# Kernel tuning notes

Measured on AMD Instinct MI355X. Metric: run time of the kernel, lower is better.

The kernel has to match this reference:

```python
import jax, jax.numpy as jnp
import numpy as np

H, K, V, F = 8, 64, 192, 192  # heads, key_size, value_size, num_position_features


def central_mask_features(distances, feature_size, seq_length):
    # distances: [L] float; returns [L, feature_size]
    pow_rate = np.exp(np.log(seq_length + 1) / feature_size).astype('float32')
    center_widths = jnp.power(pow_rate, jnp.arange(1, feature_size + 1, dtype=jnp.float32)) - 1.0
    return (center_widths[None, :] > jnp.abs(distances)[:, None]).astype(jnp.float32)


def positional_features(distances, feature_size, seq_length, symmetric=False):
    num_components = 1 if symmetric else 2
    emb = central_mask_features(distances, feature_size // num_components, seq_length)
    if not symmetric:
        emb = jnp.concatenate([emb, jnp.sign(distances)[:, None] * emb], axis=-1)
    return emb  # [L, feature_size]


def relative_shift(x):
    # x: [B, H, T1, T2] with T2 = 2*T1 - 1 -> [B, H, T1, T1]
    b, h, t1, t2 = x.shape
    x = jnp.pad(x, ((0, 0), (0, 0), (0, 0), (1, 0)))  # [B,H,T1,T2+1]
    x = x.reshape(b, h, t2 + 1, t1)[:, :, 1:, :]      # drop first row
    x = x.reshape(b, h, t1, t2)
    return x[..., : (t2 + 1) // 2]


def setup_inputs() -> dict:
    key = jax.random.key(0)
    ks = jax.random.split(key, 9)
    B, T, C = 2, 1536, 1536
    s = 1.0 / np.sqrt(C).astype('float32')
    return {
        'inputs': jax.random.normal(ks[0], (B, T, C), jnp.float32),
        'Wq': jax.random.normal(ks[1], (C, H * K), jnp.float32) * s,
        'Wk': jax.random.normal(ks[2], (C, H * K), jnp.float32) * s,
        'Wv': jax.random.normal(ks[3], (C, H * V), jnp.float32) * s,
        'Wrk': jax.random.normal(ks[4], (F, H * K), jnp.float32) * (1.0 / np.sqrt(F).astype('float32')),
        'We': jax.random.normal(ks[5], (H * V, H * V), jnp.float32) * (1.0 / np.sqrt(H * V).astype('float32')),
        'be': jnp.zeros((H * V,), jnp.float32),
        'r_w_bias': jax.random.normal(ks[6], (1, H, 1, K), jnp.float32) * 0.1,
        'r_r_bias': jax.random.normal(ks[7], (1, H, 1, K), jnp.float32) * 0.1,
    }


def reference(inputs, Wq, Wk, Wv, Wrk, We, be, r_w_bias, r_r_bias):
    B, T, C = inputs.shape

    def heads(x, d):  # [B,T,H*d] -> [B,H,T,d]
        return x.reshape(B, T, H, d).transpose(0, 2, 1, 3)

    q = heads(inputs @ Wq, K) * (K ** -0.5)
    k = heads(inputs @ Wk, K)
    v = heads(inputs @ Wv, V)

    # content logits: (q + r_w_bias) k^T -> [B,H,T,T]
    content_logits = jnp.einsum('bhqk,bhmk->bhqm', q + r_w_bias, k)

    # relative position logits
    distances = jnp.arange(-T + 1, T, dtype=jnp.float32)  # [2T-1]
    pe = positional_features(distances, F, T, symmetric=False)  # [2T-1, F]
    r_k = (pe @ Wrk).reshape(2 * T - 1, H, K).transpose(1, 0, 2)  # [H, 2T-1, K]
    rel_logits = jnp.einsum('bhqk,hmk->bhqm', q + r_r_bias, r_k)  # [B,H,T,2T-1]
    rel_logits = relative_shift(rel_logits)  # [B,H,T,T]

    logits = content_logits + rel_logits
    attn = jax.nn.softmax(logits, axis=-1)
    out = jnp.einsum('bhqm,bhmv->bhqv', attn, v)  # [B,H,T,V]
    out = out.transpose(0, 2, 1, 3).reshape(B, T, H * V)
    return out @ We + be
```

## Files before the change

### kernel.cpp

```cpp
#include <hip/hip_runtime.h>
#include <math.h>

#define HB 8
#define KD 64
#define VD 192
#define BT 2
#define TT 1536
#define CC 1536
#define HK (HB*KD)
#define HV (HB*VD)
#define QKVP 2560

typedef float f32x4 __attribute__((ext_vector_type(4)));
typedef __bf16 bf16x8 __attribute__((ext_vector_type(8)));
typedef uint uint2v __attribute__((ext_vector_type(2)));

static __device__ __forceinline__ ushort f2bf(float f) {
  union { float f; uint u; } v; v.f = f;
  uint r = (v.u + 0x7FFFu + ((v.u >> 16) & 1u)) >> 16;
  return (ushort)r;
}
static __device__ __forceinline__ float bf2f(ushort u) {
  union { uint u; float f; } v; v.u = ((uint)u) << 16; return v.f;
}

static __device__ __forceinline__ f32x4 mfma_bf(bf16x8 a, bf16x8 b, f32x4 c) {
  return __builtin_amdgcn_mfma_f32_16x16x32_bf16(a, b, c, 0, 0, 0);
}

static __device__ __forceinline__ void gload_lds16(const ushort* g, ushort* l) {
  __builtin_amdgcn_global_load_lds(
      (const __attribute__((address_space(1))) unsigned int*)g,
      (__attribute__((address_space(3))) unsigned int*)l, 16, 0, 0);
}

__device__ __forceinline__ void storeC(float* p, float v) { *p = v; }
__device__ __forceinline__ void storeC(ushort* p, float v) { *p = f2bf(v); }

__global__ __launch_bounds__(256) void cast_bf16(
    const float* __restrict__ in, ushort* __restrict__ out, int n4)
{
  for (int i = blockIdx.x*blockDim.x + threadIdx.x; i < n4; i += gridDim.x*blockDim.x) {
    float4 v = ((const float4*)in)[i];
    ushort4 o; o.x = f2bf(v.x); o.y = f2bf(v.y); o.z = f2bf(v.z); o.w = f2bf(v.w);
    ((ushort4*)out)[i] = o;
  }
}

__global__ void tcast(const float* __restrict__ in, ushort* __restrict__ out, int R, int C, float scale)
{
  __shared__ float tile[32][33];
  const int bx = blockIdx.x * 32;
  const int by = blockIdx.y * 32;
  const int tx = threadIdx.x, ty = threadIdx.y;
  #pragma unroll
  for (int i = 0; i < 4; ++i)
    tile[ty + i*8][tx] = in[(size_t)(by + ty + i*8)*C + bx + tx];
  __syncthreads();
  #pragma unroll
  for (int i = 0; i < 4; ++i)
    out[(size_t)(bx + ty + i*8)*R + by + tx] = f2bf(tile[tx][ty + i*8] * scale);
}

__global__ void vtrans(const ushort* __restrict__ in, ushort* __restrict__ out)
{
  __shared__ ushort tile[32][33];
  const int bx = blockIdx.x * 32;
  const int by = blockIdx.y * 32;
  const int tx = threadIdx.x, ty = threadIdx.y;
  #pragma unroll
  for (int i = 0; i < 4; ++i)
    tile[ty + i*8][tx] = in[(size_t)(by + ty + i*8)*QKVP + 1024 + bx + tx];
  __syncthreads();
  #pragma unroll
  for (int i = 0; i < 4; ++i)
    out[(size_t)(bx + ty + i*8)*(BT*TT) + by + tx] = tile[tx][ty + i*8];
}

template<bool WITH_BIAS, typename OutT>
__global__ __launch_bounds__(256) void gemm_bf16(
    const ushort* __restrict__ A, const ushort* __restrict__ Bt,
    const float* __restrict__ bias, OutT* __restrict__ C,
    int M, int N, int Kd)
{
  __shared__ __align__(16) ushort As[128*64];
  __shared__ __align__(16) ushort Bs[128*64];
  const int t = threadIdx.x;
  const int w = t >> 6, lane = t & 63;
  const int lrow = lane & 15, lk8 = lane >> 4;
  const int row0 = blockIdx.y * 128, col0 = blockIdx.x * 128;
  const int wr = (w >> 1) * 64, wc = (w & 1) * 64;

  f32x4 acc[4][4];
  #pragma unroll
  for (int m = 0; m < 4; ++m)
    #pragma unroll
    for (int n = 0; n < 4; ++n) acc[m][n] = (f32x4){0.f,0.f,0.f,0.f};

  for (int k0 = 0; k0 < Kd; k0 += 64) {
    __syncthreads();
    #pragma unroll
    for (int j = 0; j < 4; ++j) {
      const int c = (w*4 + j)*64 + lane;
      const int r = c >> 3, cp = c & 7;
      const int sc = cp ^ (r & 7);
      gload_lds16(A  + (size_t)(row0 + r)*Kd + k0 + sc*8, As + c*8);
      gload_lds16(Bt + (size_t)(col0 + r)*Kd + k0 + sc*8, Bs + c*8);
    }
    __syncthreads();
    bf16x8 af[4][2], bfv[4][2];
    #pragma unroll
    for (int m = 0; m < 4; ++m) {
      const int r = wr + m*16 + lrow;
      #pragma unroll
      for (int kh = 0; kh < 2; ++kh) {
        const int k8 = lk8 + kh*4;
        af[m][kh] = *(const bf16x8*)&As[r*64 + ((k8 ^ (r & 7)) << 3)];
      }
    }
    #pragma unroll
    for (int n = 0; n < 4; ++n) {
      const int r = wc + n*16 + lrow;
      #pragma unroll
      for (int kh = 0; kh < 2; ++kh) {
        const int k8 = lk8 + kh*4;
        bfv[n][kh] = *(const bf16x8*)&Bs[r*64 + ((k8 ^ (r & 7)) << 3)];
      }
    }
    #pragma unroll
    for (int m = 0; m < 4; ++m)
      #pragma unroll
      for (int n = 0; n < 4; ++n) {
        acc[m][n] = mfma_bf(af[m][0], bfv[n][0], acc[m][n]);
        acc[m][n] = mfma_bf(af[m][1], bfv[n][1], acc[m][n]);
      }
  }
  #pragma unroll
  for (int m = 0; m < 4; ++m)
    #pragma unroll
    for (int n = 0; n < 4; ++n) {
      const int cg = col0 + wc + n*16 + lrow;
      const float bb = WITH_BIAS ? bias[cg] : 0.f;
      #pragma unroll
      for (int r = 0; r < 4; ++r) {
        const int rg = row0 + wr + m*16 + lk8*4 + r;
        storeC(&C[(size_t)rg*N + cg], acc[m][n][r] + bb);
      }
    }
}

__global__ __launch_bounds__(256) void wrk_suffix(
    const float* __restrict__ Wrk, float* __restrict__ S1, float* __restrict__ S2)
{
  const int c = blockIdx.x*blockDim.x + threadIdx.x;
  float a1 = 0.f, a2 = 0.f;
  S1[96*HK + c] = 0.f; S2[96*HK + c] = 0.f;
  for (int i = 95; i >= 0; --i) {
    a1 += Wrk[i*HK + c];
    a2 += Wrk[(96 + i)*HK + c];
    S1[i*HK + c] = a1; S2[i*HK + c] = a2;
  }
}

__global__ __launch_bounds__(256) void relk_fill(
    const float* __restrict__ S1, const float* __restrict__ S2,
    const float* __restrict__ rrb, ushort* __restrict__ rk, float* __restrict__ c2g)
{
  __shared__ float cw[96];
  __shared__ float red[512];
  __shared__ int i0s;
  const int t = threadIdx.x;
  const int m = blockIdx.x;
  if (t < 96) {
    double pr = exp(log((double)(TT + 1)) / 96.0);
    float prf = (float)pr;
    cw[t] = (float)pow((double)prf, (double)(t + 1)) - 1.0f;
  }
  __syncthreads();
  const int d = m - (TT - 1);
  const float ad = fabsf((float)d);
  if (t == 0) {
    int i0 = 96;
    for (int i = 0; i < 96; ++i) if (cw[i] > ad) { i0 = i; break; }
    i0s = i0;
  }
  __syncthreads();
  const float sg = (d > 0) ? 1.f : (d < 0 ? -1.f : 0.f);
  const int i0 = i0s;
  for (int c = t; c < HK; c += 256) {
    const float val = S1[i0*HK + c] + sg * S2[i0*HK + c];
    const ushort vb = f2bf(val);
    rk[(size_t)m * HK + c] = vb;
    red[c] = bf2f(vb) * rrb[c];
  }
  __syncthreads();
  if (t < 8) {
    float s = 0.f;
    #pragma unroll 16
    for (int i = 0; i < 64; ++i) s += red[t*64 + i];
    c2g[(size_t)t*(2*TT - 1) + m] = s;
  }
}

__global__ __launch_bounds__(256) void c1_kernel(
    const ushort* __restrict__ qkv, const float* __restrict__ rwb, float* __restrict__ c1g)
{
  const int idx = blockIdx.x*256 + threadIdx.x;
  const int h = idx & 7, row = idx >> 3;
  const ushort* kr = &qkv[(size_t)row*QKVP + 512 + h*KD];
  float s = 0.f;
  #pragma unroll 16
  for (int c = 0; c < 64; ++c) s += bf2f(kr[c]) * rwb[h*KD + c];
  c1g[h*(BT*TT) + row] = s;
}

__global__ __launch_bounds__(256) void attn_mfma(
    const ushort* __restrict__ qkv, const ushort* __restrict__ vTg,
    const ushort* __restrict__ rk,
    const float* __restrict__ c1g, const float* __restrict__ c2g,
    ushort* __restrict__ aout)
{
  __shared__ __align__(16) ushort ktL[32*64];
  __shared__ __align__(16) ushort rkbL[64*64];
  __shared__ __align__(16) ushort vTl[192*64];
  __shared__ __align__(16) ushort Pl[32][40];
  __shared__ __align__(16) float S1[32][33];
  __shared__ __align__(16) float S2[32][66];
  __shared__ float c1s[32], c2s[64];
  __shared__ float corrl[32], linv[32];

  const int t = threadIdx.x;
  const int wv = t >> 6, lane = t & 63;
  const int lrow = lane & 15, lk8 = lane >> 4;
  const int bid = blockIdx.x;
  const int qt = bid % (TT/32);
  const int h  = (bid / (TT/32)) % HB;
  const int b  = bid / ((TT/32) * HB);
  const int q0 = qt * 32;

  bf16x8 af[2][2];
  #pragma unroll
  for (int rt = 0; rt < 2; ++rt)
    #pragma unroll
    for (int kh = 0; kh < 2; ++kh)
      af[rt][kh] = *(const bf16x8*)&qkv[((size_t)(b*TT) + q0 + rt*16 + lrow)*QKVP + h*KD + kh*32 + lk8*8];

  if (t < 32) ((uint*)rkbL)[63*32 + t] = 0;

  const int kc_r = t >> 3, kc_p = t & 7;
  const ushort* ksrc = qkv + (size_t)(b*TT + kc_r)*QKVP + 512 + h*KD + (kc_p ^ (kc_r & 7))*8;
  ushort* kdst = ktL + t*8;
  const ushort* rsrc[2]; ushort* rdst[2];
  #pragma unroll
  for (int W = 0; W < 2; ++W) {
    const int c = W*256 + t;
    const int rr = c >> 3, cp = c & 7;
    rsrc[W] = rk + (size_t)(TT - 32 - q0 + rr)*HK + h*KD + (cp ^ (rr & 7))*8;
    rdst[W] = rkbL + c*8;
  }
  const bool rval = t < 248;
  const ushort* vsrc[6]; ushort* vdst[6];
  #pragma unroll
  for (int W = 0; W < 6; ++W) {
    const int c = W*256 + t;
    const int vd = c >> 3, cpk = c & 7;
    vsrc[W] = vTg + (size_t)(h*VD + vd)*(BT*TT) + b*TT + (cpk ^ (vd & 7))*8;
    vdst[W] = vTl + c*8;
  }

  f32x4 acc[2][3];
  #pragma unroll
  for (int i = 0; i < 2; ++i)
    #pragma unroll
    for (int j = 0; j < 3; ++j) acc[i][j] = (f32x4){0.f, 0.f, 0.f, 0.f};
  float m_i = -1e30f, l_i = 0.f;
  const int r_s = t >> 3;
  const int vsl = t & 7;

  for (int kt0 = 0; kt0 < TT; kt0 += 32) {
    __syncthreads();
    gload_lds16(ksrc, kdst);                 ksrc += 32*QKVP;
    gload_lds16(rsrc[0], rdst[0]);           rsrc[0] += 32*HK;
    if (rval) gload_lds16(rsrc[1], rdst[1]); rsrc[1] += 32*HK;
    if ((kt0 & 32) == 0) {
      #pragma unroll
      for (int W = 0; W < 6; ++W) { gload_lds16(vsrc[W], vdst[W]); vsrc[W] += 64; }
    }
    const int mbase = kt0 - q0 + (TT - 32);
    if (t < 32) c1s[t] = c1g[h*(BT*TT) + b*TT + kt0 + t];
    else if (t >= 64 && t < 128) {
      const int m = t - 64;
      c2s[m] = (m < 63) ? c2g[(size_t)h*(2*TT - 1) + mbase + m] : 0.f;
    }
    asm volatile("s_waitcnt vmcnt(0)" ::: "memory");
    __syncthreads();
    {
      const int rt = wv >> 1, ct = wv & 1;
      const int jk = ct*16 + lrow;
      bf16x8 b0 = *(const bf16x8*)&ktL[jk*64 + ((lk8 ^ (jk & 7)) << 3)];
      bf16x8 b1 = *(const bf16x8*)&ktL[jk*64 + (((lk8 + 4) ^ (jk & 7)) << 3)];
      f32x4 c0 = (f32x4){0.f, 0.f, 0.f, 0.f};
      c0 = mfma_bf(af[rt][0], b0, c0);
      c0 = mfma_bf(af[rt][1], b1, c0);
      const float cadd = c1s[jk];
      #pragma unroll
      for (int r = 0; r < 4; ++r) S1[rt*16 + lk8*4 + r][jk] = c0[r] + cadd;
    }
    #pragma unroll
    for (int s2 = 0; s2 < 2; ++s2) {
      const int rt = wv >> 1, ct = (wv & 1)*2 + s2;
      const int j2 = ct*16 + lrow;
      bf16x8 b0 = *(const bf16x8*)&rkbL[j2*64 + ((lk8 ^ (j2 & 7)) << 3)];
      bf16x8 b1 = *(const bf16x8*)&rkbL[j2*64 + (((lk8 + 4) ^ (j2 & 7)) << 3)];
      f32x4 c0 = (f32x4){0.f, 0.f, 0.f, 0.f};
      c0 = mfma_bf(af[rt][0], b0, c0);
      c0 = mfma_bf(af[rt][1], b1, c0);
      const float cadd = c2s[j2];
      #pragma unroll
      for (int r = 0; r < 4; ++r) S2[rt*16 + lk8*4 + r][j2] = c0[r] + cadd;
    }
    __syncthreads();
    {
      float sv[4];
      #pragma unroll
      for (int i = 0; i < 4; ++i) {
        const int j = vsl*4 + i;
        sv[i] = S1[r_s][j] + S2[r_s][j - r_s + 31];
      }
      float lmax = fmaxf(fmaxf(sv[0], sv[1]), fmaxf(sv[2], sv[3]));
      #pragma unroll
      for (int s = 1; s < 8; s <<= 1) lmax = fmaxf(lmax, __shfl_xor(lmax, s, 64));
      const float m_new = fmaxf(m_i, lmax);
      const float corr = __expf(m_i - m_new);
      const float p0 = __expf(sv[0] - m_new), p1 = __expf(sv[1] - m_new);
      const float p2 = __expf(sv[2] - m_new), p3 = __expf(sv[3] - m_new);
      uint2v pw;
      pw.x = (uint)f2bf(p0) | ((uint)f2bf(p1) << 16);
      pw.y = (uint)f2bf(p2) | ((uint)f2bf(p3) << 16);
      *(uint2v*)&Pl[r_s][vsl*4] = pw;
      float lsum = (p0 + p1) + (p2 + p3);
      #pragma unroll
      for (int s = 1; s < 8; s <<= 1) lsum += __shfl_xor(lsum, s, 64);
      l_i = l_i * corr + lsum;
      m_i = m_new;
      if (vsl == 0) corrl[r_s] = corr;
    }
    __syncthreads();
    {
      const int kh4 = ((kt0 >> 5) & 1) * 4;
      float cr[2][4];
      #pragma unroll
      for (int rt = 0; rt < 2; ++rt)
        #pragma unroll
        for (int r = 0; r < 4; ++r) cr[rt][r] = corrl[rt*16 + lk8*4 + r];
      #pragma unroll
      for (int rt = 0; rt < 2; ++rt) {
        const bf16x8 pa = *(const bf16x8*)&Pl[rt*16 + lrow][lk8*8];
        #pragma unroll
        for (int cc = 0; cc < 3; ++cc) {
          const int rv = (3*wv + cc)*16 + lrow;
          const bf16x8 bv = *(const bf16x8*)&vTl[rv*64 + (((kh4 + lk8) ^ (rv & 7)) << 3)];
          f32x4 a = acc[rt][cc];
          #pragma unroll
          for (int r = 0; r < 4; ++r) a[r] *= cr[rt][r];
          acc[rt][cc] = mfma_bf(pa, bv, a);
        }
      }
    }
  }
  if (vsl == 0) linv[r_s] = 1.0f / l_i;
  __syncthreads();
  #pragma unroll
  for (int rt = 0; rt < 2; ++rt) {
    #pragma unroll
    for (int cc = 0; cc < 3; ++cc) {
      const int colg = (3*wv + cc)*16 + lrow;
      #pragma unroll
      for (int r = 0; r < 4; ++r) {
        const int rowg = rt*16 + lk8*4 + r;
        aout[((size_t)(b*TT) + q0 + rowg) * HV + h*VD + colg] = f2bf(acc[rt][cc][r] * linv[rowg]);
      }
    }
  }
}

extern "C" void kernel_launch(void* const* d_in, const int* in_sizes, int n_in,
                              void* d_out, int out_size, void* d_ws, size_t ws_size,
                              hipStream_t stream)
{
  const float* X   = (const float*)d_in[0];
  const float* Wq  = (const float*)d_in[1];
  const float* Wk  = (const float*)d_in[2];
  const float* Wv  = (const float*)d_in[3];
  const float* Wrk = (const float*)d_in[4];
  const float* We  = (const float*)d_in[5];
  const float* be  = (const float*)d_in[6];
  const float* rwb = (const float*)d_in[7];
  const float* rrb = (const float*)d_in[8];
  float* out = (float*)d_out;

  char* ws = (char*)d_ws;
  ushort* Xb    = (ushort*)ws;                       ws += (size_t)3072*1536*2;
  ushort* Wqkvt = (ushort*)ws;                       ws += (size_t)2560*1536*2;
  ushort* Wet   = (ushort*)ws;                       ws += (size_t)1536*1536*2;
  float*  S1b   = (float*)ws;                        ws += (size_t)97*512*4;
  float*  S2b   = (float*)ws;                        ws += (size_t)97*512*4;
  ushort* qkvb  = (ushort*)ws;                       ws += (size_t)3072*2560*2;
  ushort* vTgb  = (ushort*)ws;                       ws += (size_t)1536*3072*2;
  ushort* rkb   = (ushort*)ws;                       ws += (size_t)3071*512*2;
  float*  c1g   = (float*)ws;                        ws += (size_t)8*3072*4;
  float*  c2g   = (float*)ws;                        ws += (size_t)8*3071*4;
  ushort* ao    = (ushort*)ws;

  dim3 blk(256);
  cast_bf16<<<2048, blk, 0, stream>>>(X, Xb, (3072*1536)/4);
  tcast<<<dim3(512/32, 1536/32),  dim3(32,8), 0, stream>>>(Wq, Wqkvt,                      1536, 512,  0.125f);
  tcast<<<dim3(512/32, 1536/32),  dim3(32,8), 0, stream>>>(Wk, Wqkvt + (size_t)512*1536,   1536, 512,  1.0f);
  tcast<<<dim3(1536/32, 1536/32), dim3(32,8), 0, stream>>>(Wv, Wqkvt + (size_t)1024*1536,  1536, 1536, 1.0f);
  tcast<<<dim3(1536/32, 1536/32), dim3(32,8), 0, stream>>>(We, Wet, 1536, 1536, 1.0f);
  wrk_suffix<<<2, blk, 0, stream>>>(Wrk, S1b, S2b);
  relk_fill<<<dim3(2*TT - 1), blk, 0, stream>>>(S1b, S2b, rrb, rkb, c2g);
  gemm_bf16<false, ushort><<<dim3(20, 24), blk, 0, stream>>>(Xb, Wqkvt, nullptr, qkvb, 3072, QKVP, 1536);
  vtrans<<<dim3(1536/32, 3072/32), dim3(32,8), 0, stream>>>(qkvb, vTgb);
  c1_kernel<<<96, blk, 0, stream>>>(qkvb, rwb, c1g);
  attn_mfma<<<dim3(BT*HB*(TT/32)), blk, 0, stream>>>(qkvb, vTgb, rkb, c1g, c2g, ao);
  gemm_bf16<true, float><<<dim3(12, 24), blk, 0, stream>>>(ao, Wet, be, out, 3072, 1536, 1536);
}
```

Measured before the change: 226.0 us.

## Prefetch next K/rel-K tiles during softmax and defer softmax rescaling

Restructures the attention loop so the next key and relative-key tiles are issued right after the score MFMAs. Partial vmcnt waits let those loads overlap the softmax and PV stages, and raw s_barrier replaces the full __syncthreads. The c1/c2 bias terms are read directly into registers instead of being staged through LDS. Log2(e) is folded into the Q weights and biases so the kernel can use exp2f, and the running max is updated lazily (threshold 8), with the accumulator rescale skipped when no row changed. The lazy max lets the bf16 probabilities grow up to 2^8 before rescaling, and the hand-written waitcnt counts must match the issued load counts exactly.

```diff
diff --git a/kernel.cpp b/kernel.cpp
--- a/kernel.cpp
+++ b/kernel.cpp
@@ -10,6 +10,7 @@
 #define HK (HB*KD)
 #define HV (HB*VD)
 #define QKVP 2560
+#define LOG2E 1.44269504088896340736f
 
 typedef float f32x4 __attribute__((ext_vector_type(4)));
 typedef __bf16 bf16x8 __attribute__((ext_vector_type(8)));
@@ -198,7 +199,7 @@
     float s = 0.f;
     #pragma unroll 16
     for (int i = 0; i < 64; ++i) s += red[t*64 + i];
-    c2g[(size_t)t*(2*TT - 1) + m] = s;
+    c2g[(size_t)t*(2*TT - 1) + m] = s * LOG2E;
   }
 }
 
@@ -211,7 +212,7 @@
   float s = 0.f;
   #pragma unroll 16
   for (int c = 0; c < 64; ++c) s += bf2f(kr[c]) * rwb[h*KD + c];
-  c1g[h*(BT*TT) + row] = s;
+  c1g[h*(BT*TT) + row] = s * LOG2E;
 }
 
 __global__ __launch_bounds__(256) void attn_mfma(
@@ -224,9 +225,8 @@
   __shared__ __align__(16) ushort rkbL[64*64];
   __shared__ __align__(16) ushort vTl[192*64];
   __shared__ __align__(16) ushort Pl[32][40];
-  __shared__ __align__(16) float S1[32][33];
+  __shared__ __align__(16) float S1[32][34];
   __shared__ __align__(16) float S2[32][66];
-  __shared__ float c1s[32], c2s[64];
   __shared__ float corrl[32], linv[32];
 
   const int t = threadIdx.x;
@@ -250,14 +250,12 @@
   const int kc_r = t >> 3, kc_p = t & 7;
   const ushort* ksrc = qkv + (size_t)(b*TT + kc_r)*QKVP + 512 + h*KD + (kc_p ^ (kc_r & 7))*8;
   ushort* kdst = ktL + t*8;
-  const ushort* rsrc[2]; ushort* rdst[2];
-  #pragma unroll
-  for (int W = 0; W < 2; ++W) {
-    const int c = W*256 + t;
-    const int rr = c >> 3, cp = c & 7;
-    rsrc[W] = rk + (size_t)(TT - 32 - q0 + rr)*HK + h*KD + (cp ^ (rr & 7))*8;
-    rdst[W] = rkbL + c*8;
-  }
+  const int rr0 = t >> 3, rp0 = t & 7;
+  const int rr1 = (256 + t) >> 3, rp1 = t & 7;
+  const ushort* rsrc0 = rk + (size_t)(TT - 32 - q0 + rr0)*HK + h*KD + (rp0 ^ (rr0 & 7))*8;
+  const ushort* rsrc1 = rk + (size_t)(TT - 32 - q0 + rr1)*HK + h*KD + (rp1 ^ (rr1 & 7))*8;
+  ushort* rdst0 = rkbL + t*8;
+  ushort* rdst1 = rkbL + (256 + t)*8;
   const bool rval = t < 248;
   const ushort* vsrc[6]; ushort* vdst[6];
   #pragma unroll
@@ -268,6 +266,11 @@
     vdst[W] = vTl + c*8;
   }
 
+  const int jk  = (wv & 1)*16 + lrow;
+  const int j2a = (wv & 1)*32 + lrow;
+  const int j2b = j2a + 16;
+  const int rt_ = wv >> 1;
+
   f32x4 acc[2][3];
   #pragma unroll
   for (int i = 0; i < 2; ++i)
@@ -277,49 +280,64 @@
   const int r_s = t >> 3;
   const int vsl = t & 7;
 
-  for (int kt0 = 0; kt0 < TT; kt0 += 32) {
-    __syncthreads();
-    gload_lds16(ksrc, kdst);                 ksrc += 32*QKVP;
-    gload_lds16(rsrc[0], rdst[0]);           rsrc[0] += 32*HK;
-    if (rval) gload_lds16(rsrc[1], rdst[1]); rsrc[1] += 32*HK;
-    if ((kt0 & 32) == 0) {
+  gload_lds16(ksrc, kdst);               ksrc += 32*QKVP;
+  gload_lds16(rsrc0, rdst0);             rsrc0 += 32*HK;
+  if (rval) gload_lds16(rsrc1, rdst1);
+  rsrc1 += 32*HK;
+
+  for (int it = 0; it < 48; ++it) {
+    const int kt0 = it << 5;
+    const int mbase = kt0 - q0 + (TT - 32);
+    const float c1v  = c1g[h*(BT*TT) + b*TT + kt0 + jk];
+    const float c2v0 = c2g[(size_t)h*(2*TT - 1) + mbase + j2a];
+    const float c2r  = c2g[(size_t)h*(2*TT - 1) + mbase + (j2b < 63 ? j2b : 62)];
+    const float c2v1 = (j2b < 63) ? c2r : 0.f;
+
+    if ((it & 1) == 0) {
+      asm volatile("s_waitcnt lgkmcnt(0)" ::: "memory");
+      __builtin_amdgcn_s_barrier();
       #pragma unroll
       for (int W = 0; W < 6; ++W) { gload_lds16(vsrc[W], vdst[W]); vsrc[W] += 64; }
-    }
-    const int mbase = kt0 - q0 + (TT - 32);
-    if (t < 32) c1s[t] = c1g[h*(BT*TT) + b*TT + kt0 + t];
-    else if (t >= 64 && t < 128) {
-      const int m = t - 64;
-      c2s[m] = (m < 63) ? c2g[(size_t)h*(2*TT - 1) + mbase + m] : 0.f;
-    }
-    asm volatile("s_waitcnt vmcnt(0)" ::: "memory");
-    __syncthreads();
+      asm volatile("s_waitcnt vmcnt(6)" ::: "memory");
+      __builtin_amdgcn_s_barrier();
+    } else {
+      asm volatile("s_waitcnt vmcnt(3)" ::: "memory");
+      __builtin_amdgcn_s_barrier();
+    }
+
     {
-      const int rt = wv >> 1, ct = wv & 1;
-      const int jk = ct*16 + lrow;
       bf16x8 b0 = *(const bf16x8*)&ktL[jk*64 + ((lk8 ^ (jk & 7)) << 3)];
       bf16x8 b1 = *(const bf16x8*)&ktL[jk*64 + (((lk8 + 4) ^ (jk & 7)) << 3)];
       f32x4 c0 = (f32x4){0.f, 0.f, 0.f, 0.f};
-      c0 = mfma_bf(af[rt][0], b0, c0);
-      c0 = mfma_bf(af[rt][1], b1, c0);
-      const float cadd = c1s[jk];
-      #pragma unroll
-      for (int r = 0; r < 4; ++r) S1[rt*16 + lk8*4 + r][jk] = c0[r] + cadd;
-    }
-    #pragma unroll
-    for (int s2 = 0; s2 < 2; ++s2) {
-      const int rt = wv >> 1, ct = (wv & 1)*2 + s2;
-      const int j2 = ct*16 + lrow;
-      bf16x8 b0 = *(const bf16x8*)&rkbL[j2*64 + ((lk8 ^ (j2 & 7)) << 3)];
-      bf16x8 b1 = *(const bf16x8*)&rkbL[j2*64 + (((lk8 + 4) ^ (j2 & 7)) << 3)];
-      f32x4 c0 = (f32x4){0.f, 0.f, 0.f, 0.f};
-      c0 = mfma_bf(af[rt][0], b0, c0);
-      c0 = mfma_bf(af[rt][1], b1, c0);
-      const float cadd = c2s[j2];
-      #pragma unroll
-      for (int r = 0; r < 4; ++r) S2[rt*16 + lk8*4 + r][j2] = c0[r] + cadd;
-    }
-    __syncthreads();
+      c0 = mfma_bf(af[rt_][0], b0, c0);
+      c0 = mfma_bf(af[rt_][1], b1, c0);
+      #pragma unroll
+      for (int r = 0; r < 4; ++r) S1[rt_*16 + lk8*4 + r][jk] = c0[r] + c1v;
+
+      bf16x8 d0 = *(const bf16x8*)&rkbL[j2a*64 + ((lk8 ^ (j2a & 7)) << 3)];
+      bf16x8 d1 = *(const bf16x8*)&rkbL[j2a*64 + (((lk8 + 4) ^ (j2a & 7)) << 3)];
+      f32x4 ca = (f32x4){0.f, 0.f, 0.f, 0.f};
+      ca = mfma_bf(af[rt_][0], d0, ca);
+      ca = mfma_bf(af[rt_][1], d1, ca);
+      #pragma unroll
+      for (int r = 0; r < 4; ++r) S2[rt_*16 + lk8*4 + r][j2a] = ca[r] + c2v0;
+
+      bf16x8 e0 = *(const bf16x8*)&rkbL[j2b*64 + ((lk8 ^ (j2b & 7)) << 3)];
+      bf16x8 e1 = *(const bf16x8*)&rkbL[j2b*64 + (((lk8 + 4) ^ (j2b & 7)) << 3)];
+      f32x4 cb = (f32x4){0.f, 0.f, 0.f, 0.f};
+      cb = mfma_bf(af[rt_][0], e0, cb);
+      cb = mfma_bf(af[rt_][1], e1, cb);
+      #pragma unroll
+      for (int r = 0; r < 4; ++r) S2[rt_*16 + lk8*4 + r][j2b] = cb[r] + c2v1;
+    }
+    asm volatile("s_waitcnt lgkmcnt(0)" ::: "memory");
+    __builtin_amdgcn_s_barrier();
+    if (it < 47) {
+      gload_lds16(ksrc, kdst);               ksrc += 32*QKVP;
+      gload_lds16(rsrc0, rdst0);             rsrc0 += 32*HK;
+      if (rval) gload_lds16(rsrc1, rdst1);
+      rsrc1 += 32*HK;
+    }
     {
       float sv[4];
       #pragma unroll
@@ -330,10 +348,11 @@
       float lmax = fmaxf(fmaxf(sv[0], sv[1]), fmaxf(sv[2], sv[3]));
       #pragma unroll
       for (int s = 1; s < 8; s <<= 1) lmax = fmaxf(lmax, __shfl_xor(lmax, s, 64));
-      const float m_new = fmaxf(m_i, lmax);
-      const float corr = __expf(m_i - m_new);
-      const float p0 = __expf(sv[0] - m_new), p1 = __expf(sv[1] - m_new);
-      const float p2 = __expf(sv[2] - m_new), p3 = __expf(sv[3] - m_new);
+      const bool defer = (lmax <= m_i + 8.0f);
+      const float m_new = defer ? m_i : fmaxf(m_i, lmax);
+      const float corr  = defer ? 1.0f : exp2f(m_i - m_new);
+      const float p0 = exp2f(sv[0] - m_new), p1 = exp2f(sv[1] - m_new);
+      const float p2 = exp2f(sv[2] - m_new), p3 = exp2f(sv[3] - m_new);
       uint2v pw;
       pw.x = (uint)f2bf(p0) | ((uint)f2bf(p1) << 16);
       pw.y = (uint)f2bf(p2) | ((uint)f2bf(p3) << 16);
@@ -345,14 +364,29 @@
       m_i = m_new;
       if (vsl == 0) corrl[r_s] = corr;
     }
-    __syncthreads();
+    if ((it & 1) == 0) { asm volatile("s_waitcnt vmcnt(3)" ::: "memory"); }
+    asm volatile("s_waitcnt lgkmcnt(0)" ::: "memory");
+    __builtin_amdgcn_s_barrier();
     {
-      const int kh4 = ((kt0 >> 5) & 1) * 4;
+      const int kh4 = (it & 1) * 4;
       float cr[2][4];
       #pragma unroll
       for (int rt = 0; rt < 2; ++rt)
         #pragma unroll
         for (int r = 0; r < 4; ++r) cr[rt][r] = corrl[rt*16 + lk8*4 + r];
+      bool need = false;
+      #pragma unroll
+      for (int rt = 0; rt < 2; ++rt)
+        #pragma unroll
+        for (int r = 0; r < 4; ++r) need |= (cr[rt][r] != 1.0f);
+      if (__any(need ? 1 : 0)) {
+        #pragma unroll
+        for (int rt = 0; rt < 2; ++rt)
+          #pragma unroll
+          for (int cc = 0; cc < 3; ++cc)
+            #pragma unroll
+            for (int r = 0; r < 4; ++r) acc[rt][cc][r] *= cr[rt][r];
+      }
       #pragma unroll
       for (int rt = 0; rt < 2; ++rt) {
         const bf16x8 pa = *(const bf16x8*)&Pl[rt*16 + lrow][lk8*8];
@@ -360,10 +394,7 @@
         for (int cc = 0; cc < 3; ++cc) {
           const int rv = (3*wv + cc)*16 + lrow;
           const bf16x8 bv = *(const bf16x8*)&vTl[rv*64 + (((kh4 + lk8) ^ (rv & 7)) << 3)];
-          f32x4 a = acc[rt][cc];
-          #pragma unroll
-          for (int r = 0; r < 4; ++r) a[r] *= cr[rt][r];
-          acc[rt][cc] = mfma_bf(pa, bv, a);
+          acc[rt][cc] = mfma_bf(pa, bv, acc[rt][cc]);
         }
       }
     }
@@ -414,7 +445,7 @@
 
   dim3 blk(256);
   cast_bf16<<<2048, blk, 0, stream>>>(X, Xb, (3072*1536)/4);
-  tcast<<<dim3(512/32, 1536/32),  dim3(32,8), 0, stream>>>(Wq, Wqkvt,                      1536, 512,  0.125f);
+  tcast<<<dim3(512/32, 1536/32),  dim3(32,8), 0, stream>>>(Wq, Wqkvt,                      1536, 512,  0.125f*LOG2E);
   tcast<<<dim3(512/32, 1536/32),  dim3(32,8), 0, stream>>>(Wk, Wqkvt + (size_t)512*1536,   1536, 512,  1.0f);
   tcast<<<dim3(1536/32, 1536/32), dim3(32,8), 0, stream>>>(Wv, Wqkvt + (size_t)1024*1536,  1536, 1536, 1.0f);
   tcast<<<dim3(1536/32, 1536/32), dim3(32,8), 0, stream>>>(We, Wet, 1536, 1536, 1.0f);
```

New measurement: 224.1 us. About the same (-0.8%).
